# Kernel tuning notes

Hardware: AMD Instinct MI355X
Metric: run time of the kernel (lower is better)

Reference implementation:

```python
import jax, jax.numpy as jnp
import numpy as np

N, E = 50000, 800000
IN, HID, OUT = 256, 128, 64


def setup_inputs() -> dict:
    key = jax.random.key(0)
    ks = jax.random.split(key, 8)
    x = jax.random.normal(ks[0], (N, IN), dtype=jnp.float32)
    edge_index = jax.random.randint(ks[1], (2, E), 0, N, dtype=jnp.int64)
    # PyG GCNConv: Linear weight [out, in] (glorot-ish), bias [out] (zeros init; use small randn for a nontrivial baseline)
    W1 = jax.random.normal(ks[2], (HID, IN), dtype=jnp.float32) / np.sqrt(IN)
    b1 = jax.random.normal(ks[3], (HID,), dtype=jnp.float32) * 0.01
    Wmu = jax.random.normal(ks[4], (OUT, HID), dtype=jnp.float32) / np.sqrt(HID)
    bmu = jax.random.normal(ks[5], (OUT,), dtype=jnp.float32) * 0.01
    Wlv = jax.random.normal(ks[6], (OUT, HID), dtype=jnp.float32) / np.sqrt(HID)
    blv = jax.random.normal(ks[7], (OUT,), dtype=jnp.float32) * 0.01
    return {"x": x, "edge_index": edge_index, "W1": W1, "b1": b1,
            "Wmu": Wmu, "bmu": bmu, "Wlv": Wlv, "blv": blv}


def reference(x, edge_index, W1, b1, Wmu, bmu, Wlv, blv):
    n = x.shape[0]
    loop = jnp.arange(n, dtype=edge_index.dtype)
    src = jnp.concatenate([edge_index[0], loop])  # [E+N]
    dst = jnp.concatenate([edge_index[1], loop])
    # symmetric normalization with self-loops: deg computed on destinations
    deg = jax.ops.segment_sum(jnp.ones_like(dst, dtype=x.dtype), dst, num_segments=n)
    dis = jax.lax.rsqrt(deg)  # deg >= 1 due to self-loops
    norm = dis[src] * dis[dst]  # [E+N]

    def gcn(h, W, b):
        hw = h @ W.T                                   # [N, out]
        msg = hw[src] * norm[:, None]                  # [E+N, out] gather + scale
        return jax.ops.segment_sum(msg, dst, num_segments=n) + b

    h = jax.nn.relu(gcn(x, W1, b1))
    # dropout(p=0.5) is identity in eval mode
    return (gcn(h, Wmu, bmu), gcn(h, Wlv, blv))
```

## Files before the change

### kernel.cpp

```cpp
#include <hip/hip_runtime.h>

#define N_NODES 50000
#define N_EDGES 800000
#define DIN 256
#define DHID 128
#define DOUT 64
#define NB_SCAN 49
#define SENT N_NODES

typedef __attribute__((ext_vector_type(8))) short short8;
typedef __attribute__((ext_vector_type(4))) float f32x4;

static __device__ __forceinline__ short f2bf(float f) {
    union { float f; unsigned u; } v; v.f = f;
    unsigned r = v.u + 0x7FFFu + ((v.u >> 16) & 1u);
    return (short)(r >> 16);
}
static __device__ __forceinline__ float bflo(unsigned p) {
    union { unsigned u; float f; } v; v.u = p << 16; return v.f;
}
static __device__ __forceinline__ float bfhi(unsigned p) {
    union { unsigned u; float f; } v; v.u = p & 0xFFFF0000u; return v.f;
}
static __device__ __forceinline__ unsigned pk(float lo, float hi) {
    return ((unsigned)(unsigned short)f2bf(lo)) |
           (((unsigned)(unsigned short)f2bf(hi)) << 16);
}


__global__ void count_kernel(const int* __restrict__ ei, int* __restrict__ cnt,
                             int* __restrict__ loc) {
    int stride = gridDim.x * blockDim.x;
    for (int e = blockIdx.x * blockDim.x + threadIdx.x; e < N_EDGES; e += stride) {
        loc[e] = atomicAdd(&cnt[ei[N_EDGES + e]], 1);
    }
}

__global__ __launch_bounds__(1024) void bsum_kernel(const int* __restrict__ cnt,
                                                    int* __restrict__ bsum) {
    __shared__ int ws[16];
    int tid = threadIdx.x, i = blockIdx.x * 1024 + tid;
    int v = (i < N_NODES) ? cnt[i] : 0;
    v = (v + 7) & ~7;
    #pragma unroll
    for (int off = 32; off >= 1; off >>= 1) v += __shfl_xor(v, off);
    if ((tid & 63) == 0) ws[tid >> 6] = v;
    __syncthreads();
    if (tid == 0) {
        int s = 0;
        #pragma unroll
        for (int w = 0; w < 16; ++w) s += ws[w];
        bsum[blockIdx.x] = s;
    }
}

__global__ void bscan_kernel(const int* __restrict__ bsum, int* __restrict__ bo,
                             int* __restrict__ rowptr) {
    int l = threadIdx.x;
    int v = (l < NB_SCAN) ? bsum[l] : 0;
    int x = v;
    #pragma unroll
    for (int off = 1; off < 64; off <<= 1) {
        int y = __shfl_up(x, off);
        if (l >= off) x += y;
    }
    if (l < NB_SCAN) bo[l] = x - v;
    if (l == 63) rowptr[N_NODES] = x;
}

__global__ __launch_bounds__(1024) void scan_apply_kernel(const int* __restrict__ cnt,
        const int* __restrict__ bo, int* __restrict__ rowptr,
        float* __restrict__ dis, int* __restrict__ col) {
    __shared__ int wsum[16];
    int tid = threadIdx.x, i = blockIdx.x * 1024 + tid;
    int lane = tid & 63, wid = tid >> 6;
    int v = (i < N_NODES) ? cnt[i] : 0;
    int p = (v + 7) & ~7;
    int x = p;
    #pragma unroll
    for (int off = 1; off < 64; off <<= 1) {
        int y = __shfl_up(x, off);
        if (lane >= off) x += y;
    }
    if (lane == 63) wsum[wid] = x;
    __syncthreads();
    if (tid == 0) {
        int s = 0;
        #pragma unroll
        for (int w = 0; w < 16; ++w) { int t = wsum[w]; wsum[w] = s; s += t; }
    }
    __syncthreads();
    int excl = bo[blockIdx.x] + wsum[wid] + (x - p);
    if (i < N_NODES) {
        rowptr[i] = excl;
        dis[i] = rsqrtf((float)(v + 1));
        for (int q = v; q < p; ++q) col[excl + q] = SENT;
    }
}

__global__ void fill_kernel(const int* __restrict__ ei, const int* __restrict__ loc,
                            const int* __restrict__ rowptr, int* __restrict__ col) {
    int stride = gridDim.x * blockDim.x;
    for (int e = blockIdx.x * blockDim.x + threadIdx.x; e < N_EDGES; e += stride) {
        int s = ei[e];
        int d = ei[N_EDGES + e];
        col[rowptr[d] + loc[e]] = s;
    }
}


__global__ void wprep_kernel(const float* __restrict__ W1, const float* __restrict__ Wmu,
                             const float* __restrict__ Wlv, short* __restrict__ W1b,
                             short* __restrict__ Wctb, short* __restrict__ u1b,
                             short* __restrict__ u2b) {
    int tid = blockIdx.x * blockDim.x + threadIdx.x;
    if (tid < DHID * DIN) {
        W1b[tid] = f2bf(W1[tid]);
    } else if (tid < DHID * DIN + 2 * DOUT * DHID) {
        int t = tid - DHID * DIN;
        Wctb[t] = f2bf((t < DOUT * DHID) ? Wmu[t] : Wlv[t - DOUT * DHID]);
    } else if (tid < DHID * DIN + 2 * DOUT * DHID + DHID) {
        int t = tid - (DHID * DIN + 2 * DOUT * DHID);
        u1b[(size_t)SENT * DHID + t] = 0;
        u2b[(size_t)SENT * DHID + t] = 0;
    }
}


__global__ __launch_bounds__(256) void xprep_kernel(const float* __restrict__ x,
        const float* __restrict__ dis, short* __restrict__ xb) {
    const int total = N_NODES * (DIN / 8);
    int stride = gridDim.x * blockDim.x;
    for (int c = blockIdx.x * blockDim.x + threadIdx.x; c < total; c += stride) {
        int row = c >> 5;
        float d = dis[row];
        const float* src = x + (size_t)c * 8;
        float4 f0 = *(const float4*)src;
        float4 f1 = *(const float4*)(src + 4);
        short8 o;
        o[0] = f2bf(f0.x * d); o[1] = f2bf(f0.y * d);
        o[2] = f2bf(f0.z * d); o[3] = f2bf(f0.w * d);
        o[4] = f2bf(f1.x * d); o[5] = f2bf(f1.y * d);
        o[6] = f2bf(f1.z * d); o[7] = f2bf(f1.w * d);
        *(short8*)(xb + (size_t)c * 8) = o;
    }
}


__global__ __launch_bounds__(256) void gemm1_mfma_kernel(const short* __restrict__ xb,
        const short* __restrict__ W1b, short* __restrict__ u1b) {
    const int lane = threadIdx.x & 63, w = threadIdx.x >> 6;
    const int l15 = lane & 15, kg = lane >> 4;
    const int nb = blockIdx.x * 64;
    const int r0 = nb + w * 16 + l15;
    const bool valid = r0 < N_NODES;
    const short* arow = xb + (size_t)r0 * DIN;

    f32x4 acc[8] = {};
    #pragma unroll
    for (int ks = 0; ks < 8; ++ks) {
        const int k0 = ks * 32 + kg * 8;
        short8 a = valid ? *(const short8*)(arow + k0)
                         : short8{0, 0, 0, 0, 0, 0, 0, 0};
        #pragma unroll
        for (int c = 0; c < 8; ++c) {
            short8 b = *(const short8*)(W1b + (size_t)(c * 16 + l15) * DIN + k0);
            acc[c] = __builtin_amdgcn_mfma_f32_16x16x32_bf16(a, b, acc[c], 0, 0, 0);
        }
    }

    const int rb = nb + w * 16 + kg * 4;
    #pragma unroll
    for (int c = 0; c < 8; ++c) {
        const int j = c * 16 + l15;
        #pragma unroll
        for (int e = 0; e < 4; ++e) {
            int r = rb + e;
            if (r < N_NODES)
                u1b[(size_t)r * DHID + j] = f2bf(acc[c][e]);
        }
    }
}


template <bool LAYER1>
__global__ __launch_bounds__(256) void pull_kernel(const int* __restrict__ rowptr,
        const int* __restrict__ col, const short* __restrict__ uin,
        const float* __restrict__ dis, const float* __restrict__ b1,
        unsigned* __restrict__ uout) {
    const int wid = threadIdx.x >> 6, lane = threadIdx.x & 63;
    const int g = lane >> 4, j = lane & 15;
    const int i = blockIdx.x * 4 + wid;
    if (i >= N_NODES) return;
    const int beg = rowptr[i], end = rowptr[i + 1];
    const uint4* __restrict__ up4 = (const uint4*)uin;
    float a0 = 0.f, a1 = 0.f, a2 = 0.f, a3 = 0.f;
    float a4 = 0.f, a5 = 0.f, a6 = 0.f, a7 = 0.f;
    for (int base = beg; base < end; base += 64) {
        const int rem = end - base;
        const int m = rem < 64 ? rem : 64;
        int cv = (lane < m) ? col[base + lane] : SENT;
        for (int t = 0; t < m; t += 8) {
            int c0 = __shfl(cv, t + g);
            int c1 = __shfl(cv, t + 4 + g);
            uint4 v0 = up4[(size_t)c0 * 16 + j];
            uint4 v1 = up4[(size_t)c1 * 16 + j];
            a0 += bflo(v0.x); a1 += bfhi(v0.x);
            a2 += bflo(v0.y); a3 += bfhi(v0.y);
            a4 += bflo(v0.z); a5 += bfhi(v0.z);
            a6 += bflo(v0.w); a7 += bfhi(v0.w);
            a0 += bflo(v1.x); a1 += bfhi(v1.x);
            a2 += bflo(v1.y); a3 += bfhi(v1.y);
            a4 += bflo(v1.z); a5 += bfhi(v1.z);
            a6 += bflo(v1.w); a7 += bfhi(v1.w);
        }
    }
    a0 += __shfl_xor(a0, 16); a0 += __shfl_xor(a0, 32);
    a1 += __shfl_xor(a1, 16); a1 += __shfl_xor(a1, 32);
    a2 += __shfl_xor(a2, 16); a2 += __shfl_xor(a2, 32);
    a3 += __shfl_xor(a3, 16); a3 += __shfl_xor(a3, 32);
    a4 += __shfl_xor(a4, 16); a4 += __shfl_xor(a4, 32);
    a5 += __shfl_xor(a5, 16); a5 += __shfl_xor(a5, 32);
    a6 += __shfl_xor(a6, 16); a6 += __shfl_xor(a6, 32);
    a7 += __shfl_xor(a7, 16); a7 += __shfl_xor(a7, 32);

    const uint4 sv = up4[(size_t)i * 16 + j];
    const float di = dis[i];
    float t0 = di * (a0 + bflo(sv.x));
    float t1 = di * (a1 + bfhi(sv.x));
    float t2 = di * (a2 + bflo(sv.y));
    float t3 = di * (a3 + bfhi(sv.y));
    float t4 = di * (a4 + bflo(sv.z));
    float t5 = di * (a5 + bfhi(sv.z));
    float t6 = di * (a6 + bflo(sv.w));
    float t7 = di * (a7 + bfhi(sv.w));
    if (LAYER1) {
        float4 bl = *(const float4*)(b1 + j * 8);
        float4 bh = *(const float4*)(b1 + j * 8 + 4);
        t0 = fmaxf(t0 + bl.x, 0.f) * di;
        t1 = fmaxf(t1 + bl.y, 0.f) * di;
        t2 = fmaxf(t2 + bl.z, 0.f) * di;
        t3 = fmaxf(t3 + bl.w, 0.f) * di;
        t4 = fmaxf(t4 + bh.x, 0.f) * di;
        t5 = fmaxf(t5 + bh.y, 0.f) * di;
        t6 = fmaxf(t6 + bh.z, 0.f) * di;
        t7 = fmaxf(t7 + bh.w, 0.f) * di;
    }
    if (g == 0) {
        uint4 o;
        o.x = pk(t0, t1);
        o.y = pk(t2, t3);
        o.z = pk(t4, t5);
        o.w = pk(t6, t7);
        ((uint4*)uout)[(size_t)i * 16 + j] = o;
    }
}


__global__ __launch_bounds__(256) void gemm2_mfma_kernel(const short* __restrict__ a2b,
        const short* __restrict__ Wctb, const float* __restrict__ bmu,
        const float* __restrict__ blv, float* __restrict__ out) {
    const int lane = threadIdx.x & 63, w = threadIdx.x >> 6;
    const int l15 = lane & 15, kg = lane >> 4;
    const int nb = blockIdx.x * 64;
    const int r0 = nb + w * 16 + l15;
    const bool valid = r0 < N_NODES;
    const short* arow = a2b + (size_t)r0 * DHID;

    f32x4 acc[8] = {};
    #pragma unroll
    for (int ks = 0; ks < 4; ++ks) {
        const int k0 = ks * 32 + kg * 8;
        short8 a = valid ? *(const short8*)(arow + k0)
                         : short8{0, 0, 0, 0, 0, 0, 0, 0};
        #pragma unroll
        for (int c = 0; c < 8; ++c) {
            short8 b = *(const short8*)(Wctb + (size_t)(c * 16 + l15) * DHID + k0);
            acc[c] = __builtin_amdgcn_mfma_f32_16x16x32_bf16(a, b, acc[c], 0, 0, 0);
        }
    }

    float bias[8];
    #pragma unroll
    for (int c = 0; c < 8; ++c) {
        int j = c * 16 + l15;
        bias[c] = (j < DOUT) ? bmu[j] : blv[j - DOUT];
    }
    const int rb = nb + w * 16 + kg * 4;
    #pragma unroll
    for (int c = 0; c < 8; ++c) {
        const int j = c * 16 + l15;
        float* dst = (j < DOUT) ? (out + j)
                                : (out + (size_t)N_NODES * DOUT + (j - DOUT));
        #pragma unroll
        for (int e = 0; e < 4; ++e) {
            int r = rb + e;
            if (r < N_NODES)
                dst[(size_t)r * DOUT] = acc[c][e] + bias[c];
        }
    }
}


extern "C" void kernel_launch(void* const* d_in, const int* in_sizes, int n_in,
                              void* d_out, int out_size, void* d_ws, size_t ws_size,
                              hipStream_t stream) {
    const float* x   = (const float*)d_in[0];
    const int*   ei  = (const int*)d_in[1];
    const float* W1  = (const float*)d_in[2];
    const float* b1  = (const float*)d_in[3];
    const float* Wmu = (const float*)d_in[4];
    const float* bmu = (const float*)d_in[5];
    const float* Wlv = (const float*)d_in[6];
    const float* blv = (const float*)d_in[7];
    float* out = (float*)d_out;

    char* ws = (char*)d_ws;
    size_t off = 0;
    auto alloc = [&](size_t bytes) -> char* {
        char* p = ws + off;
        off += (bytes + 255) & ~(size_t)255;
        return p;
    };
    const size_t COL_CAP = (size_t)N_EDGES + 8 * (size_t)N_NODES + 64;
    int*   cnt    = (int*)  alloc((size_t)N_NODES * 4);
    int*   rowptr = (int*)  alloc((size_t)(N_NODES + 1) * 4);
    float* dis    = (float*)alloc((size_t)N_NODES * 4);
    int*   loc    = (int*)  alloc((size_t)N_EDGES * 4);
    int*   col    = (int*)  alloc(COL_CAP * 4);
    int*   bsum   = (int*)  alloc((size_t)NB_SCAN * 4);
    int*   bo     = (int*)  alloc((size_t)NB_SCAN * 4);
    short* W1b    = (short*)alloc((size_t)DHID * DIN * 2);
    short* Wctb   = (short*)alloc((size_t)2 * DOUT * DHID * 2);
    short* xb     = (short*)alloc((size_t)N_NODES * DIN * 2);
    short* u1b    = (short*)alloc((size_t)(N_NODES + 1) * DHID * 2);
    short* u2b    = (short*)alloc((size_t)(N_NODES + 1) * DHID * 2);
    short* a2b    = u1b;

    hipMemsetAsync(cnt, 0, (size_t)N_NODES * 4, stream);
    wprep_kernel<<<193, 256, 0, stream>>>(W1, Wmu, Wlv, W1b, Wctb, u1b, u2b);
    count_kernel<<<1024, 256, 0, stream>>>(ei, cnt, loc);
    bsum_kernel<<<NB_SCAN, 1024, 0, stream>>>(cnt, bsum);
    bscan_kernel<<<1, 64, 0, stream>>>(bsum, bo, rowptr);
    scan_apply_kernel<<<NB_SCAN, 1024, 0, stream>>>(cnt, bo, rowptr, dis, col);
    fill_kernel<<<1024, 256, 0, stream>>>(ei, loc, rowptr, col);
    xprep_kernel<<<2048, 256, 0, stream>>>(x, dis, xb);
    gemm1_mfma_kernel<<<(N_NODES + 63) / 64, 256, 0, stream>>>(xb, W1b, u1b);
    pull_kernel<true><<<N_NODES / 4, 256, 0, stream>>>(rowptr, col, u1b, dis, b1,
                                                       (unsigned*)u2b);
    pull_kernel<false><<<N_NODES / 4, 256, 0, stream>>>(rowptr, col, u2b, dis, nullptr,
                                                        (unsigned*)a2b);
    gemm2_mfma_kernel<<<(N_NODES + 63) / 64, 256, 0, stream>>>(a2b, Wctb, bmu, blv, out);
}
```

Before: 282.8 us.

## Merge prep kernels and overlap CSR fill with GEMM1 via block partitioning

Scaling x by dis moves from before the GEMM to the GEMM1 epilogue (row scaling commutes with the matmul). The x-to-bf16 conversion therefore no longer depends on the degree scan and can run in one horizontally fused kernel together with edge counting and weight prep. The CSR fill and GEMM1 are likewise merged into a single launch with disjoint block ranges, so the bandwidth-bound scatter overlaps with the MFMA work. This removes several launches and serialization points, at the cost of fixed block splits and a slightly different bf16 rounding point.

```diff
diff --git a/kernel.cpp b/kernel.cpp
--- a/kernel.cpp
+++ b/kernel.cpp
@@ -8,6 +8,12 @@
 #define NB_SCAN 49
 #define SENT N_NODES
 
+#define MP_XPREP_BLOCKS 640
+#define MP_COUNT_BLOCKS 320
+#define MP_WPREP_BLOCKS 64
+#define FG_GEMM_BLOCKS 782
+#define FG_FILL_BLOCKS 242
+
 typedef __attribute__((ext_vector_type(8))) short short8;
 typedef __attribute__((ext_vector_type(4))) float f32x4;
 
@@ -28,13 +34,52 @@
 }
 
 
-__global__ void count_kernel(const int* __restrict__ ei, int* __restrict__ cnt,
-                             int* __restrict__ loc) {
-    int stride = gridDim.x * blockDim.x;
-    for (int e = blockIdx.x * blockDim.x + threadIdx.x; e < N_EDGES; e += stride) {
-        loc[e] = atomicAdd(&cnt[ei[N_EDGES + e]], 1);
-    }
-}
+__global__ __launch_bounds__(256) void mega_prep_kernel(
+        const float* __restrict__ x, short* __restrict__ xb,
+        const int* __restrict__ ei, int* __restrict__ cnt, int* __restrict__ loc,
+        const float* __restrict__ W1, const float* __restrict__ Wmu,
+        const float* __restrict__ Wlv, short* __restrict__ W1b,
+        short* __restrict__ Wctb, short* __restrict__ u1b, short* __restrict__ u2b) {
+    const int b = blockIdx.x;
+    if (b < MP_XPREP_BLOCKS) {
+        const int total = N_NODES * (DIN / 8);
+        const int stride = MP_XPREP_BLOCKS * 256;
+        for (int c = b * 256 + threadIdx.x; c < total; c += stride) {
+            const float* src = x + (size_t)c * 8;
+            float4 f0 = *(const float4*)src;
+            float4 f1 = *(const float4*)(src + 4);
+            short8 o;
+            o[0] = f2bf(f0.x); o[1] = f2bf(f0.y);
+            o[2] = f2bf(f0.z); o[3] = f2bf(f0.w);
+            o[4] = f2bf(f1.x); o[5] = f2bf(f1.y);
+            o[6] = f2bf(f1.z); o[7] = f2bf(f1.w);
+            *(short8*)(xb + (size_t)c * 8) = o;
+        }
+    } else if (b < MP_XPREP_BLOCKS + MP_COUNT_BLOCKS) {
+        const int stride = MP_COUNT_BLOCKS * 256;
+        for (int e = (b - MP_XPREP_BLOCKS) * 256 + threadIdx.x; e < N_EDGES;
+             e += stride) {
+            loc[e] = atomicAdd(&cnt[ei[N_EDGES + e]], 1);
+        }
+    } else {
+        const int TOT = DHID * DIN + 2 * DOUT * DHID + DHID;
+        const int stride = MP_WPREP_BLOCKS * 256;
+        for (int t = (b - MP_XPREP_BLOCKS - MP_COUNT_BLOCKS) * 256 + threadIdx.x;
+             t < TOT; t += stride) {
+            if (t < DHID * DIN) {
+                W1b[t] = f2bf(W1[t]);
+            } else if (t < DHID * DIN + 2 * DOUT * DHID) {
+                int u = t - DHID * DIN;
+                Wctb[u] = f2bf((u < DOUT * DHID) ? Wmu[u] : Wlv[u - DOUT * DHID]);
+            } else {
+                int s = t - (DHID * DIN + 2 * DOUT * DHID);
+                u1b[(size_t)SENT * DHID + s] = 0;
+                u2b[(size_t)SENT * DHID + s] = 0;
+            }
+        }
+    }
+}
+
 
 __global__ __launch_bounds__(1024) void bsum_kernel(const int* __restrict__ cnt,
                                                     int* __restrict__ bsum) {
@@ -98,86 +143,55 @@
     }
 }
 
-__global__ void fill_kernel(const int* __restrict__ ei, const int* __restrict__ loc,
-                            const int* __restrict__ rowptr, int* __restrict__ col) {
-    int stride = gridDim.x * blockDim.x;
-    for (int e = blockIdx.x * blockDim.x + threadIdx.x; e < N_EDGES; e += stride) {
-        int s = ei[e];
-        int d = ei[N_EDGES + e];
-        col[rowptr[d] + loc[e]] = s;
-    }
-}
-
-
-__global__ void wprep_kernel(const float* __restrict__ W1, const float* __restrict__ Wmu,
-                             const float* __restrict__ Wlv, short* __restrict__ W1b,
-                             short* __restrict__ Wctb, short* __restrict__ u1b,
-                             short* __restrict__ u2b) {
-    int tid = blockIdx.x * blockDim.x + threadIdx.x;
-    if (tid < DHID * DIN) {
-        W1b[tid] = f2bf(W1[tid]);
-    } else if (tid < DHID * DIN + 2 * DOUT * DHID) {
-        int t = tid - DHID * DIN;
-        Wctb[t] = f2bf((t < DOUT * DHID) ? Wmu[t] : Wlv[t - DOUT * DHID]);
-    } else if (tid < DHID * DIN + 2 * DOUT * DHID + DHID) {
-        int t = tid - (DHID * DIN + 2 * DOUT * DHID);
-        u1b[(size_t)SENT * DHID + t] = 0;
-        u2b[(size_t)SENT * DHID + t] = 0;
-    }
-}
-
-
-__global__ __launch_bounds__(256) void xprep_kernel(const float* __restrict__ x,
-        const float* __restrict__ dis, short* __restrict__ xb) {
-    const int total = N_NODES * (DIN / 8);
-    int stride = gridDim.x * blockDim.x;
-    for (int c = blockIdx.x * blockDim.x + threadIdx.x; c < total; c += stride) {
-        int row = c >> 5;
-        float d = dis[row];
-        const float* src = x + (size_t)c * 8;
-        float4 f0 = *(const float4*)src;
-        float4 f1 = *(const float4*)(src + 4);
-        short8 o;
-        o[0] = f2bf(f0.x * d); o[1] = f2bf(f0.y * d);
-        o[2] = f2bf(f0.z * d); o[3] = f2bf(f0.w * d);
-        o[4] = f2bf(f1.x * d); o[5] = f2bf(f1.y * d);
-        o[6] = f2bf(f1.z * d); o[7] = f2bf(f1.w * d);
-        *(short8*)(xb + (size_t)c * 8) = o;
-    }
-}
-
-
-__global__ __launch_bounds__(256) void gemm1_mfma_kernel(const short* __restrict__ xb,
-        const short* __restrict__ W1b, short* __restrict__ u1b) {
-    const int lane = threadIdx.x & 63, w = threadIdx.x >> 6;
-    const int l15 = lane & 15, kg = lane >> 4;
-    const int nb = blockIdx.x * 64;
-    const int r0 = nb + w * 16 + l15;
-    const bool valid = r0 < N_NODES;
-    const short* arow = xb + (size_t)r0 * DIN;
-
-    f32x4 acc[8] = {};
-    #pragma unroll
-    for (int ks = 0; ks < 8; ++ks) {
-        const int k0 = ks * 32 + kg * 8;
-        short8 a = valid ? *(const short8*)(arow + k0)
-                         : short8{0, 0, 0, 0, 0, 0, 0, 0};
+
+__global__ __launch_bounds__(256) void fill_gemm1_kernel(
+        const int* __restrict__ ei, const int* __restrict__ loc,
+        const int* __restrict__ rowptr, int* __restrict__ col,
+        const short* __restrict__ xb, const short* __restrict__ W1b,
+        const float* __restrict__ dis, short* __restrict__ u1b) {
+    const int b = blockIdx.x;
+    if (b < FG_GEMM_BLOCKS) {
+        const int lane = threadIdx.x & 63, w = threadIdx.x >> 6;
+        const int l15 = lane & 15, kg = lane >> 4;
+        const int nb = b * 64;
+        const int r0 = nb + w * 16 + l15;
+        const bool valid = r0 < N_NODES;
+        const short* arow = xb + (size_t)r0 * DIN;
+
+        f32x4 acc[8] = {};
+        #pragma unroll
+        for (int ks = 0; ks < 8; ++ks) {
+            const int k0 = ks * 32 + kg * 8;
+            short8 a = valid ? *(const short8*)(arow + k0)
+                             : short8{0, 0, 0, 0, 0, 0, 0, 0};
+            #pragma unroll
+            for (int c = 0; c < 8; ++c) {
+                short8 bb = *(const short8*)(W1b + (size_t)(c * 16 + l15) * DIN + k0);
+                acc[c] = __builtin_amdgcn_mfma_f32_16x16x32_bf16(a, bb, acc[c], 0, 0, 0);
+            }
+        }
+
+        const int rb = nb + w * 16 + kg * 4;
+        float dv[4];
+        #pragma unroll
+        for (int e = 0; e < 4; ++e) dv[e] = (rb + e < N_NODES) ? dis[rb + e] : 0.f;
         #pragma unroll
         for (int c = 0; c < 8; ++c) {
-            short8 b = *(const short8*)(W1b + (size_t)(c * 16 + l15) * DIN + k0);
-            acc[c] = __builtin_amdgcn_mfma_f32_16x16x32_bf16(a, b, acc[c], 0, 0, 0);
-        }
-    }
-
-    const int rb = nb + w * 16 + kg * 4;
-    #pragma unroll
-    for (int c = 0; c < 8; ++c) {
-        const int j = c * 16 + l15;
-        #pragma unroll
-        for (int e = 0; e < 4; ++e) {
-            int r = rb + e;
-            if (r < N_NODES)
-                u1b[(size_t)r * DHID + j] = f2bf(acc[c][e]);
+            const int j = c * 16 + l15;
+            #pragma unroll
+            for (int e = 0; e < 4; ++e) {
+                int r = rb + e;
+                if (r < N_NODES)
+                    u1b[(size_t)r * DHID + j] = f2bf(acc[c][e] * dv[e]);
+            }
+        }
+    } else {
+        const int stride = FG_FILL_BLOCKS * 256;
+        for (int e = (b - FG_GEMM_BLOCKS) * 256 + threadIdx.x; e < N_EDGES;
+             e += stride) {
+            int s = ei[e];
+            int d = ei[N_EDGES + e];
+            col[rowptr[d] + loc[e]] = s;
         }
     }
 }
@@ -338,14 +352,13 @@
     short* a2b    = u1b;
 
     hipMemsetAsync(cnt, 0, (size_t)N_NODES * 4, stream);
-    wprep_kernel<<<193, 256, 0, stream>>>(W1, Wmu, Wlv, W1b, Wctb, u1b, u2b);
-    count_kernel<<<1024, 256, 0, stream>>>(ei, cnt, loc);
+    mega_prep_kernel<<<1024, 256, 0, stream>>>(x, xb, ei, cnt, loc, W1, Wmu, Wlv,
+                                               W1b, Wctb, u1b, u2b);
     bsum_kernel<<<NB_SCAN, 1024, 0, stream>>>(cnt, bsum);
     bscan_kernel<<<1, 64, 0, stream>>>(bsum, bo, rowptr);
     scan_apply_kernel<<<NB_SCAN, 1024, 0, stream>>>(cnt, bo, rowptr, dis, col);
-    fill_kernel<<<1024, 256, 0, stream>>>(ei, loc, rowptr, col);
-    xprep_kernel<<<2048, 256, 0, stream>>>(x, dis, xb);
-    gemm1_mfma_kernel<<<(N_NODES + 63) / 64, 256, 0, stream>>>(xb, W1b, u1b);
+    fill_gemm1_kernel<<<FG_GEMM_BLOCKS + FG_FILL_BLOCKS, 256, 0, stream>>>(
+        ei, loc, rowptr, col, xb, W1b, dis, u1b);
     pull_kernel<true><<<N_NODES / 4, 256, 0, stream>>>(rowptr, col, u1b, dis, b1,
                                                        (unsigned*)u2b);
     pull_kernel<false><<<N_NODES / 4, 256, 0, stream>>>(rowptr, col, u2b, dis, nullptr,
```

After: 260.2 us. -8.0%, faster.
